# Kernel tuning notes

Measured on AMD Instinct MI355X. Metric: run time of the kernel, lower is better.

Reference implementation:

```python
import jax, jax.numpy as jnp
import numpy as np

B, D, H, E, K = 16384, 1024, 256, 8, 2
EPS = 1e-9


def setup_inputs() -> dict:
    key = jax.random.key(0)
    ks = jax.random.split(key, 4)
    scale_in = 1.0 / np.sqrt(D)
    scale_h = 1.0 / np.sqrt(H)
    return {
        "x": jax.random.normal(ks[0], (B, D), dtype=jnp.float32),
        "gate_w": jax.random.normal(ks[1], (D, E), dtype=jnp.float32) * scale_in,
        "gate_b": jnp.zeros((E,), dtype=jnp.float32),
        "w1": jax.random.normal(ks[2], (E, D, H), dtype=jnp.float32) * scale_in,
        "b1": jnp.zeros((E, H), dtype=jnp.float32),
        "w2": jax.random.normal(ks[3], (E, H, D), dtype=jnp.float32) * scale_h,
        "b2": jnp.zeros((E, D), dtype=jnp.float32),
    }


def reference(x, gate_w, gate_b, w1, b1, w2, b2):
    # Gating: logits -> softmax -> top-k mask -> renormalize (top_k_gating)
    logits = x @ gate_w + gate_b                      # [B, E]
    probs = jax.nn.softmax(logits, axis=-1)           # [B, E]
    _, topk_idx = jax.lax.top_k(probs, K)             # [B, K]
    rows = jnp.arange(probs.shape[0])[:, None]
    mask = jnp.zeros_like(probs).at[rows, topk_idx].set(1.0)
    masked = probs * mask
    denom = jnp.clip(jnp.sum(masked, axis=-1, keepdims=True), EPS, None)
    gating_weights = masked / denom                   # [B, E]

    # Dense all-experts MLP: Linear -> GELU(exact) -> Linear, batched over E
    h = jax.nn.gelu(jnp.einsum('bd,edh->beh', x, w1) + b1, approximate=False)  # [B, E, H]
    expert_outs = jnp.einsum('beh,ehd->bed', h, w2) + b2                        # [B, E, D]

    # Gating-weighted sum over experts
    output = jnp.einsum('bed,be->bd', expert_outs, gating_weights)              # [B, D]
    return output
```

## Files before the change

### kernel.cpp

```cpp
#include <hip/hip_runtime.h>
#include <stdint.h>

#define BN 16384
#define DD 1024
#define HH 256
#define EE 8
#define GB 512
#define GR 32

typedef __attribute__((ext_vector_type(8))) short short8;
typedef __attribute__((ext_vector_type(4))) float floatx4;

__device__ __forceinline__ unsigned short f2bf(float f) {
  union { float f; unsigned int i; } v; v.f = f;
  unsigned int x = v.i;
  x += 0x7fffu + ((x >> 16) & 1u);
  return (unsigned short)(x >> 16);
}
__device__ __forceinline__ unsigned int pack2(float a, float b) {
  return (unsigned int)f2bf(a) | ((unsigned int)f2bf(b) << 16);
}
__device__ __forceinline__ float bf2f(unsigned int u16) {
  union { unsigned int i; float f; } v; v.i = u16 << 16; return v.f;
}
__device__ __forceinline__ void async16(const unsigned short* g, unsigned short* l) {
  __builtin_amdgcn_global_load_lds(
      (const __attribute__((address_space(1))) void*)g,
      (__attribute__((address_space(3))) void*)l, 16, 0, 0);
}

__global__ __launch_bounds__(256) void convert_kernel(const float* __restrict__ x,
                                                      unsigned short* __restrict__ xb) {
  size_t idx = ((size_t)blockIdx.x * 256 + threadIdx.x) * 8;
  float4 f0 = *(const float4*)(x + idx);
  float4 f1 = *(const float4*)(x + idx + 4);
  uint4 o;
  o.x = pack2(f0.x, f0.y); o.y = pack2(f0.z, f0.w);
  o.z = pack2(f1.x, f1.y); o.w = pack2(f1.z, f1.w);
  *(uint4*)(xb + idx) = o;
}

__global__ __launch_bounds__(256) void gating_kernel(
    const float* __restrict__ x,
    const float* __restrict__ gate_w,
    const float* __restrict__ gate_b,
    int* __restrict__ rinfo_e, float* __restrict__ rinfo_w,
    int* __restrict__ bhist) {
  __shared__ int hist[EE];
  int tid = threadIdx.x;
  if (tid < EE) hist[tid] = 0;
  __syncthreads();
  int lane = tid & 63, wv = tid >> 6;
#pragma unroll 1
  for (int it = 0; it < GR / 4; it++) {
    int row = blockIdx.x * GR + it * 4 + wv;
    const float4* xr4 = (const float4*)(x + (size_t)row * DD);
    float acc[EE];
#pragma unroll
    for (int e = 0; e < EE; e++) acc[e] = 0.f;
#pragma unroll
    for (int i = 0; i < 4; i++) {
      int d4 = lane + i * 64;
      float4 xv = xr4[d4];
      const float4* gp = (const float4*)gate_w + (size_t)d4 * 8;
      float xs[4] = {xv.x, xv.y, xv.z, xv.w};
#pragma unroll
      for (int j = 0; j < 4; j++) {
        float4 glo = gp[2 * j], ghi = gp[2 * j + 1];
        acc[0] += xs[j] * glo.x; acc[1] += xs[j] * glo.y;
        acc[2] += xs[j] * glo.z; acc[3] += xs[j] * glo.w;
        acc[4] += xs[j] * ghi.x; acc[5] += xs[j] * ghi.y;
        acc[6] += xs[j] * ghi.z; acc[7] += xs[j] * ghi.w;
      }
    }
#pragma unroll
    for (int s = 1; s < 64; s <<= 1) {
#pragma unroll
      for (int e = 0; e < EE; e++) acc[e] += __shfl_xor(acc[e], s, 64);
    }
    if (lane == 0) {
      float lg[EE];
#pragma unroll
      for (int e = 0; e < EE; e++) lg[e] = acc[e] + gate_b[e];
      int i1 = 0;
      for (int e = 1; e < EE; e++) if (lg[e] > lg[i1]) i1 = e;
      int i2 = (i1 == 0) ? 1 : 0;
      for (int e = 0; e < EE; e++) if (e != i1 && lg[e] > lg[i2]) i2 = e;
      float wA = 1.f / (1.f + __expf(lg[i2] - lg[i1]));
      float wB = 1.f - wA;
      rinfo_e[row] = i1 | (i2 << 8);
      rinfo_w[row * 2 + 0] = wA;
      rinfo_w[row * 2 + 1] = wB;
      atomicAdd(&hist[i1], 1);
      atomicAdd(&hist[i2], 1);
    }
  }
  __syncthreads();
  if (tid < EE) bhist[blockIdx.x * EE + tid] = hist[tid];
}

__global__ __launch_bounds__(256) void scan_kernel(
    const int* __restrict__ bhist, int* __restrict__ cnt, int* __restrict__ bbase) {
  __shared__ int cs[32][EE];
  __shared__ int ofs[EE];
  int tid = threadIdx.x;
  int g = tid & 7, c = tid >> 3;
  int s = 0;
#pragma unroll 1
  for (int b = c * 16; b < c * 16 + 16; b++) s += bhist[b * EE + g];
  cs[c][g] = s;
  __syncthreads();
  if (tid == 0) {
    int run = 0;
    for (int gg = 0; gg < EE; gg++) {
      int tot = 0;
      for (int cc = 0; cc < 32; cc++) tot += cs[cc][gg];
      cnt[gg] = tot;
      cnt[32 + gg] = run;
      ofs[gg] = run;
      run += tot;
    }
  }
  __syncthreads();
  if (tid < EE) {
    int run = ofs[tid];
#pragma unroll 1
    for (int cc = 0; cc < 32; cc++) { int t = cs[cc][tid]; cs[cc][tid] = run; run += t; }
  }
  __syncthreads();
  int run = cs[c][g];
#pragma unroll 1
  for (int b = c * 16; b < c * 16 + 16; b++) {
    bbase[b * EE + g] = run;
    run += bhist[b * EE + g];
  }
}

__global__ __launch_bounds__(64) void scatter_kernel(
    const int* __restrict__ rinfo_e, const float* rinfo_w,
    const int* __restrict__ bbase,
    int* __restrict__ rowidx, float* __restrict__ wgt, int* posmap) {
  __shared__ int curs[EE];
  int tid = threadIdx.x;
  if (tid < EE) curs[tid] = bbase[blockIdx.x * EE + tid];
  __syncthreads();
  if (tid < GR) {
    int row = blockIdx.x * GR + tid;
    int ee = rinfo_e[row];
    int e0 = ee & 255, e1 = (ee >> 8) & 255;
    float w0 = rinfo_w[row * 2 + 0];
    float w1 = rinfo_w[row * 2 + 1];
    int p0 = atomicAdd(&curs[e0], 1);
    rowidx[p0] = row; wgt[p0] = w0;
    int p1 = atomicAdd(&curs[e1], 1);
    rowidx[p1] = row; wgt[p1] = w1;
    posmap[row * 2 + 0] = p0;
    posmap[row * 2 + 1] = p1;
  }
}

__global__ void transpose_kernel(const float* __restrict__ src,
                                 unsigned short* __restrict__ dst, int R, int C) {
  __shared__ float tbuf[32][33];
  int e = blockIdx.z;
  int c0 = blockIdx.x * 32, r0 = blockIdx.y * 32;
  int tx = threadIdx.x, ty = threadIdx.y;
  const float* s = src + (size_t)e * R * C;
  unsigned short* d = dst + (size_t)e * R * C;
  for (int yy = ty; yy < 32; yy += 8)
    tbuf[yy][tx] = s[(size_t)(r0 + yy) * C + c0 + tx];
  __syncthreads();
  for (int yy = ty; yy < 32; yy += 8)
    d[(size_t)(c0 + yy) * R + r0 + tx] = f2bf(tbuf[tx][yy]);
}

template <bool ASYNC_A>
__global__ __launch_bounds__(256) void gemm1_kernel(
    const unsigned short* __restrict__ xb,
    const float* __restrict__ x,
    const unsigned short* __restrict__ w1t,
    const float* __restrict__ b1,
    const int* __restrict__ cnt,
    const int* __restrict__ rowidx,
    unsigned short* __restrict__ hbuf,
    int g0, int g1) {
  __shared__ unsigned short As[128 * 64];
  __shared__ unsigned short Bs[128 * 64];
  int t = blockIdx.x, g = -1, lt = 0;
#pragma unroll 1
  for (int gg = g0; gg < g1; gg++) {
    int nt = (cnt[gg] + 127) >> 7;
    if (t < nt) { g = gg; lt = t; break; }
    t -= nt;
  }
  if (g < 0) return;
  const int* offs = cnt + 32;
  int hb = offs[g0];
  int m0 = offs[g] + lt * 128;
  int mEnd = offs[g] + cnt[g];
  int e = g;
  int n0 = blockIdx.y * 128;
  const unsigned short* Bsrc = w1t + (size_t)e * HH * DD + (size_t)n0 * DD;
  int tid = threadIdx.x, lane = tid & 63, wv = tid >> 6;
  int wr = (wv >> 1) * 64, wc = (wv & 1) * 64;
  int lm = lane & 15, q = lane >> 4;
  floatx4 acc[4][4];
  floatx4 zero = {0.f, 0.f, 0.f, 0.f};
#pragma unroll
  for (int i = 0; i < 4; i++)
#pragma unroll
    for (int j = 0; j < 4; j++) acc[i][j] = zero;
  int srow = tid >> 3;
  int scol = (tid & 7) * 8;
  const unsigned short* gA[4];
  const float* gAf[4];
  const unsigned short* gBp[4];
#pragma unroll
  for (int i = 0; i < 4; i++) {
    int pos = m0 + i * 32 + srow;
    int grow = rowidx[pos < mEnd ? pos : m0];
    if (ASYNC_A) gA[i] = xb + (size_t)grow * DD + scol;
    else         gAf[i] = x + (size_t)grow * DD + scol;
    gBp[i] = Bsrc + (size_t)(i * 32 + srow) * DD + scol;
  }
  unsigned short* AsW = As + wv * 512;
  unsigned short* BsW = Bs + wv * 512;
#pragma unroll 1
  for (int k0 = 0; k0 < DD; k0 += 64) {
    if (ASYNC_A) {
#pragma unroll
      for (int i = 0; i < 4; i++) async16(gA[i], AsW + i * 2048);
#pragma unroll
      for (int i = 0; i < 4; i++) gA[i] += 64;
    } else {
#pragma unroll
      for (int i = 0; i < 4; i++) {
        float4 f0 = *(const float4*)gAf[i];
        float4 f1 = *(const float4*)(gAf[i] + 4);
        gAf[i] += 64;
        uint4 av;
        av.x = pack2(f0.x, f0.y); av.y = pack2(f0.z, f0.w);
        av.z = pack2(f1.x, f1.y); av.w = pack2(f1.z, f1.w);
        *(uint4*)&As[(i * 32 + srow) * 64 + scol] = av;
      }
    }
#pragma unroll
    for (int i = 0; i < 4; i++) async16(gBp[i], BsW + i * 2048);
#pragma unroll
    for (int i = 0; i < 4; i++) gBp[i] += 64;
    __syncthreads();
#pragma unroll
    for (int ks = 0; ks < 2; ks++) {
      short8 a[4], b[4];
#pragma unroll
      for (int i = 0; i < 4; i++)
        a[i] = *(const short8*)&As[(wr + i * 16 + lm) * 64 + ks * 32 + q * 8];
#pragma unroll
      for (int j = 0; j < 4; j++)
        b[j] = *(const short8*)&Bs[(wc + j * 16 + lm) * 64 + ks * 32 + q * 8];
#pragma unroll
      for (int i = 0; i < 4; i++)
#pragma unroll
        for (int j = 0; j < 4; j++)
          acc[i][j] = __builtin_amdgcn_mfma_f32_16x16x32_bf16(b[j], a[i], acc[i][j], 0, 0, 0);
    }
    __syncthreads();
  }
#pragma unroll
  for (int i = 0; i < 4; i++) {
    int pos = m0 + wr + i * 16 + lm;
    if (pos < mEnd) {
#pragma unroll
      for (int j = 0; j < 4; j++) {
        int col = n0 + wc + j * 16 + q * 4;
        const float4 bb = *(const float4*)(b1 + e * HH + col);
        float v0 = acc[i][j][0] + bb.x;
        float v1 = acc[i][j][1] + bb.y;
        float v2 = acc[i][j][2] + bb.z;
        float v3 = acc[i][j][3] + bb.w;
        v0 = 0.5f * v0 * (1.f + erff(v0 * 0.70710678118654752f));
        v1 = 0.5f * v1 * (1.f + erff(v1 * 0.70710678118654752f));
        v2 = 0.5f * v2 * (1.f + erff(v2 * 0.70710678118654752f));
        v3 = 0.5f * v3 * (1.f + erff(v3 * 0.70710678118654752f));
        uint2 st; st.x = pack2(v0, v1); st.y = pack2(v2, v3);
        *(uint2*)(hbuf + (size_t)(pos - hb) * HH + col) = st;
      }
    }
  }
}

template <bool EO>
__global__ __launch_bounds__(256) void gemm2_kernel(
    const unsigned short* __restrict__ hbuf,
    const unsigned short* __restrict__ w2t,
    const float* __restrict__ b2,
    const int* __restrict__ cnt,
    const int* __restrict__ rowidx,
    const float* __restrict__ wgt,
    unsigned short* __restrict__ eo,
    float* out,
    int g0, int g1) {
  __shared__ unsigned short As[128 * 64];
  __shared__ unsigned short Bs[128 * 64];
  int t = blockIdx.x, g = -1, lt = 0;
#pragma unroll 1
  for (int gg = g0; gg < g1; gg++) {
    int nt = (cnt[gg] + 127) >> 7;
    if (t < nt) { g = gg; lt = t; break; }
    t -= nt;
  }
  if (g < 0) return;
  const int* offs = cnt + 32;
  int hb = offs[g0];
  int m0 = offs[g] + lt * 128;
  int mEnd = offs[g] + cnt[g];
  int e = g;
  int n0 = blockIdx.y * 128;
  const unsigned short* Bsrc = w2t + (size_t)e * DD * HH + (size_t)n0 * HH;
  int tid = threadIdx.x, lane = tid & 63, wv = tid >> 6;
  int wr = (wv >> 1) * 64, wc = (wv & 1) * 64;
  int lm = lane & 15, q = lane >> 4;
  floatx4 acc[4][4];
  floatx4 zero = {0.f, 0.f, 0.f, 0.f};
#pragma unroll
  for (int i = 0; i < 4; i++)
#pragma unroll
    for (int j = 0; j < 4; j++) acc[i][j] = zero;
  int srow = tid >> 3;
  int scol = (tid & 7) * 8;
  const unsigned short* gA[4];
  const unsigned short* gBp[4];
#pragma unroll
  for (int i = 0; i < 4; i++) {
    int pos = m0 + i * 32 + srow;
    int posc = (pos < mEnd) ? pos : m0;
    gA[i] = hbuf + (size_t)(posc - hb) * HH + scol;
    gBp[i] = Bsrc + (size_t)(i * 32 + srow) * HH + scol;
  }
  unsigned short* AsW = As + wv * 512;
  unsigned short* BsW = Bs + wv * 512;
#pragma unroll 1
  for (int k0 = 0; k0 < HH; k0 += 64) {
#pragma unroll
    for (int i = 0; i < 4; i++) async16(gA[i], AsW + i * 2048);
#pragma unroll
    for (int i = 0; i < 4; i++) async16(gBp[i], BsW + i * 2048);
#pragma unroll
    for (int i = 0; i < 4; i++) { gA[i] += 64; gBp[i] += 64; }
    __syncthreads();
#pragma unroll
    for (int ks = 0; ks < 2; ks++) {
      short8 a[4], b[4];
#pragma unroll
      for (int i = 0; i < 4; i++)
        a[i] = *(const short8*)&As[(wr + i * 16 + lm) * 64 + ks * 32 + q * 8];
#pragma unroll
      for (int j = 0; j < 4; j++)
        b[j] = *(const short8*)&Bs[(wc + j * 16 + lm) * 64 + ks * 32 + q * 8];
#pragma unroll
      for (int i = 0; i < 4; i++)
#pragma unroll
        for (int j = 0; j < 4; j++)
          acc[i][j] = __builtin_amdgcn_mfma_f32_16x16x32_bf16(b[j], a[i], acc[i][j], 0, 0, 0);
    }
    __syncthreads();
  }
#pragma unroll
  for (int i = 0; i < 4; i++) {
    int pos = m0 + wr + i * 16 + lm;
    if (pos < mEnd) {
      float wrow = wgt[pos];
      if (EO) {
#pragma unroll
        for (int j = 0; j < 4; j++) {
          int col = n0 + wc + j * 16 + q * 4;
          const float4 bb = *(const float4*)(b2 + e * DD + col);
          uint2 st;
          st.x = pack2((acc[i][j][0] + bb.x) * wrow, (acc[i][j][1] + bb.y) * wrow);
          st.y = pack2((acc[i][j][2] + bb.z) * wrow, (acc[i][j][3] + bb.w) * wrow);
          *(uint2*)(eo + (size_t)pos * DD + col) = st;
        }
      } else {
        int grow = rowidx[pos];
#pragma unroll
        for (int j = 0; j < 4; j++) {
          int col = n0 + wc + j * 16 + q * 4;
          const float4 bb = *(const float4*)(b2 + e * DD + col);
          float* op = out + (size_t)grow * DD + col;
          atomicAdd(op + 0, (acc[i][j][0] + bb.x) * wrow);
          atomicAdd(op + 1, (acc[i][j][1] + bb.y) * wrow);
          atomicAdd(op + 2, (acc[i][j][2] + bb.z) * wrow);
          atomicAdd(op + 3, (acc[i][j][3] + bb.w) * wrow);
        }
      }
    }
  }
}

__global__ __launch_bounds__(256) void combine_kernel(
    const unsigned short* __restrict__ eo, const int* __restrict__ posmap,
    float* __restrict__ out) {
  int row = blockIdx.x * 2 + (threadIdx.x >> 7);
  int t = threadIdx.x & 127;
  int p0 = posmap[row * 2 + 0];
  int p1 = posmap[row * 2 + 1];
  uint4 av = *((const uint4*)(eo + (size_t)p0 * DD) + t);
  uint4 bv = *((const uint4*)(eo + (size_t)p1 * DD) + t);
  unsigned int ua[4] = {av.x, av.y, av.z, av.w};
  unsigned int ub[4] = {bv.x, bv.y, bv.z, bv.w};
  float o[8];
#pragma unroll
  for (int k = 0; k < 4; k++) {
    o[2 * k]     = bf2f(ua[k] & 0xffffu) + bf2f(ub[k] & 0xffffu);
    o[2 * k + 1] = bf2f(ua[k] >> 16)     + bf2f(ub[k] >> 16);
  }
  float* op = out + (size_t)row * DD + t * 8;
  *(float4*)(op)     = make_float4(o[0], o[1], o[2], o[3]);
  *(float4*)(op + 4) = make_float4(o[4], o[5], o[6], o[7]);
}

extern "C" void kernel_launch(void* const* d_in, const int* in_sizes, int n_in,
                              void* d_out, int out_size, void* d_ws, size_t ws_size,
                              hipStream_t stream) {
  (void)in_sizes; (void)n_in; (void)out_size;
  const float* x      = (const float*)d_in[0];
  const float* gate_w = (const float*)d_in[1];
  const float* gate_b = (const float*)d_in[2];
  const float* w1     = (const float*)d_in[3];
  const float* b1     = (const float*)d_in[4];
  const float* w2     = (const float*)d_in[5];
  const float* b2     = (const float*)d_in[6];
  float* out = (float*)d_out;

  char* w = (char*)d_ws;
  int* cnt            = (int*)(w);
  int* rinfo_e        = (int*)(w + 256);
  float* rinfo_w      = (float*)(w + 65792);
  int* posmap         = (int*)(w + 65792);
  int* bhist          = (int*)(w + 196864);
  int* bbase          = (int*)(w + 229632);
  int* rowidx         = (int*)(w + 262400);
  float* wgt          = (float*)(w + 393472);
  unsigned short* w1t = (unsigned short*)(w + 524544);
  unsigned short* w2t = (unsigned short*)(w + 4718848);
  unsigned short* hbuf= (unsigned short*)(w + 8913152);
  unsigned short* xb  = (unsigned short*)(w + 25690368);
  unsigned short* eo  = (unsigned short*)(w + 59244800);
  bool fused  = ws_size >= (size_t)25690368;
  bool use_xb = ws_size >= (size_t)59244800;
  bool use_eo = ws_size >= (size_t)126353664;

  transpose_kernel<<<dim3(HH / 32, DD / 32, EE), dim3(32, 8), 0, stream>>>(w1, w1t, DD, HH);
  transpose_kernel<<<dim3(DD / 32, HH / 32, EE), dim3(32, 8), 0, stream>>>(w2, w2t, HH, DD);
  gating_kernel<<<GB, 256, 0, stream>>>(x, gate_w, gate_b, rinfo_e, rinfo_w, bhist);
  scan_kernel<<<1, 256, 0, stream>>>(bhist, cnt, bbase);
  scatter_kernel<<<GB, 64, 0, stream>>>(rinfo_e, rinfo_w, bbase, rowidx, wgt, posmap);
  if (use_eo) {
    convert_kernel<<<BN * DD / (256 * 8), 256, 0, stream>>>(x, xb);
    gemm1_kernel<true><<<dim3(264, 2), 256, 0, stream>>>(xb, x, w1t, b1, cnt, rowidx, hbuf, 0, 8);
    gemm2_kernel<true><<<dim3(264, 8), 256, 0, stream>>>(hbuf, w2t, b2, cnt, rowidx, wgt, eo, nullptr, 0, 8);
    combine_kernel<<<BN / 2, 256, 0, stream>>>(eo, posmap, out);
  } else if (use_xb) {
    hipMemsetAsync(out, 0, (size_t)BN * DD * 4, stream);
    convert_kernel<<<BN * DD / (256 * 8), 256, 0, stream>>>(x, xb);
    gemm1_kernel<true><<<dim3(264, 2), 256, 0, stream>>>(xb, x, w1t, b1, cnt, rowidx, hbuf, 0, 8);
    gemm2_kernel<false><<<dim3(264, 8), 256, 0, stream>>>(hbuf, w2t, b2, cnt, rowidx, wgt, nullptr, out, 0, 8);
  } else {
    (void)fused;
    hipMemsetAsync(out, 0, (size_t)BN * DD * 4, stream);
    gemm1_kernel<false><<<dim3(264, 2), 256, 0, stream>>>(nullptr, x, w1t, b1, cnt, rowidx, hbuf, 0, 8);
    gemm2_kernel<false><<<dim3(264, 8), 256, 0, stream>>>(hbuf, w2t, b2, cnt, rowidx, wgt, nullptr, out, 0, 8);
  }
}
```

Measured before the change: 315.7 us.

## Fuse bf16 convert into gating, double-buffer gemm1 LDS, XOR-swizzle LDS tiles

The separate fp32-to-bf16 conversion of x is folded into the gating kernel, which already reads x, so one full pass over x is removed. gemm1's async path now double-buffers the A/B shared-memory tiles, issuing the next k-tile's global-to-LDS loads before computing on the current one to overlap load latency with MFMA work. Both GEMMs use an XOR swizzle on the 16-byte column chunk, applied at the global source address and at the LDS read, to reduce bank conflicts. The cost is doubled LDS in gemm1, which may reduce occupancy, plus extra address arithmetic.

```diff
diff --git a/kernel.cpp b/kernel.cpp
--- a/kernel.cpp
+++ b/kernel.cpp
@@ -29,23 +29,13 @@
       (__attribute__((address_space(3))) void*)l, 16, 0, 0);
 }
 
-__global__ __launch_bounds__(256) void convert_kernel(const float* __restrict__ x,
-                                                      unsigned short* __restrict__ xb) {
-  size_t idx = ((size_t)blockIdx.x * 256 + threadIdx.x) * 8;
-  float4 f0 = *(const float4*)(x + idx);
-  float4 f1 = *(const float4*)(x + idx + 4);
-  uint4 o;
-  o.x = pack2(f0.x, f0.y); o.y = pack2(f0.z, f0.w);
-  o.z = pack2(f1.x, f1.y); o.w = pack2(f1.z, f1.w);
-  *(uint4*)(xb + idx) = o;
-}
-
 __global__ __launch_bounds__(256) void gating_kernel(
     const float* __restrict__ x,
     const float* __restrict__ gate_w,
     const float* __restrict__ gate_b,
     int* __restrict__ rinfo_e, float* __restrict__ rinfo_w,
-    int* __restrict__ bhist) {
+    int* __restrict__ bhist,
+    unsigned short* __restrict__ xb) {
   __shared__ int hist[EE];
   int tid = threadIdx.x;
   if (tid < EE) hist[tid] = 0;
@@ -62,6 +52,10 @@
     for (int i = 0; i < 4; i++) {
       int d4 = lane + i * 64;
       float4 xv = xr4[d4];
+      if (xb) {
+        uint2 st; st.x = pack2(xv.x, xv.y); st.y = pack2(xv.z, xv.w);
+        *(uint2*)(xb + (size_t)row * DD + (size_t)d4 * 4) = st;
+      }
       const float4* gp = (const float4*)gate_w + (size_t)d4 * 8;
       float xs[4] = {xv.x, xv.y, xv.z, xv.w};
 #pragma unroll
@@ -184,8 +178,8 @@
     const int* __restrict__ rowidx,
     unsigned short* __restrict__ hbuf,
     int g0, int g1) {
-  __shared__ unsigned short As[128 * 64];
-  __shared__ unsigned short Bs[128 * 64];
+  __shared__ unsigned short As[2][8192];
+  __shared__ unsigned short Bs[2][8192];
   int t = blockIdx.x, g = -1, lt = 0;
 #pragma unroll 1
   for (int gg = g0; gg < g1; gg++) {
@@ -204,6 +198,7 @@
   int tid = threadIdx.x, lane = tid & 63, wv = tid >> 6;
   int wr = (wv >> 1) * 64, wc = (wv & 1) * 64;
   int lm = lane & 15, q = lane >> 4;
+  int lm7 = lm & 7;
   floatx4 acc[4][4];
   floatx4 zero = {0.f, 0.f, 0.f, 0.f};
 #pragma unroll
@@ -211,7 +206,8 @@
 #pragma unroll
     for (int j = 0; j < 4; j++) acc[i][j] = zero;
   int srow = tid >> 3;
-  int scol = (tid & 7) * 8;
+  int ssrc = (((tid & 7) ^ (srow & 7))) * 8;
+  int sdst = (tid & 7) * 8;
   const unsigned short* gA[4];
   const float* gAf[4];
   const unsigned short* gBp[4];
@@ -219,20 +215,51 @@
   for (int i = 0; i < 4; i++) {
     int pos = m0 + i * 32 + srow;
     int grow = rowidx[pos < mEnd ? pos : m0];
-    if (ASYNC_A) gA[i] = xb + (size_t)grow * DD + scol;
-    else         gAf[i] = x + (size_t)grow * DD + scol;
-    gBp[i] = Bsrc + (size_t)(i * 32 + srow) * DD + scol;
-  }
-  unsigned short* AsW = As + wv * 512;
-  unsigned short* BsW = Bs + wv * 512;
-#pragma unroll 1
-  for (int k0 = 0; k0 < DD; k0 += 64) {
-    if (ASYNC_A) {
-#pragma unroll
-      for (int i = 0; i < 4; i++) async16(gA[i], AsW + i * 2048);
-#pragma unroll
-      for (int i = 0; i < 4; i++) gA[i] += 64;
-    } else {
+    if (ASYNC_A) gA[i] = xb + (size_t)grow * DD + ssrc;
+    else         gAf[i] = x + (size_t)grow * DD + ssrc;
+    gBp[i] = Bsrc + (size_t)(i * 32 + srow) * DD + ssrc;
+  }
+  auto stageAsync = [&](int bufi) {
+#pragma unroll
+    for (int i = 0; i < 4; i++) async16(gA[i], &As[bufi][wv * 512 + i * 2048]);
+#pragma unroll
+    for (int i = 0; i < 4; i++) gA[i] += 64;
+#pragma unroll
+    for (int i = 0; i < 4; i++) async16(gBp[i], &Bs[bufi][wv * 512 + i * 2048]);
+#pragma unroll
+    for (int i = 0; i < 4; i++) gBp[i] += 64;
+  };
+  auto compute = [&](int bufi) {
+#pragma unroll
+    for (int ks = 0; ks < 2; ks++) {
+      short8 a[4], b[4];
+#pragma unroll
+      for (int i = 0; i < 4; i++)
+        a[i] = *(const short8*)&As[bufi][(wr + i * 16 + lm) * 64 + ((ks * 4 + q) ^ lm7) * 8];
+#pragma unroll
+      for (int j = 0; j < 4; j++)
+        b[j] = *(const short8*)&Bs[bufi][(wc + j * 16 + lm) * 64 + ((ks * 4 + q) ^ lm7) * 8];
+#pragma unroll
+      for (int i = 0; i < 4; i++)
+#pragma unroll
+        for (int j = 0; j < 4; j++)
+          acc[i][j] = __builtin_amdgcn_mfma_f32_16x16x32_bf16(b[j], a[i], acc[i][j], 0, 0, 0);
+    }
+  };
+  if (ASYNC_A) {
+    stageAsync(0);
+    __syncthreads();
+    int buf = 0;
+#pragma unroll 1
+    for (int tt = 0; tt < DD / 64; ++tt) {
+      if (tt < DD / 64 - 1) stageAsync(buf ^ 1);
+      compute(buf);
+      __syncthreads();
+      buf ^= 1;
+    }
+  } else {
+#pragma unroll 1
+    for (int k0 = 0; k0 < DD; k0 += 64) {
 #pragma unroll
       for (int i = 0; i < 4; i++) {
         float4 f0 = *(const float4*)gAf[i];
@@ -241,30 +268,16 @@
         uint4 av;
         av.x = pack2(f0.x, f0.y); av.y = pack2(f0.z, f0.w);
         av.z = pack2(f1.x, f1.y); av.w = pack2(f1.z, f1.w);
-        *(uint4*)&As[(i * 32 + srow) * 64 + scol] = av;
+        *(uint4*)&As[0][(i * 32 + srow) * 64 + sdst] = av;
       }
-    }
-#pragma unroll
-    for (int i = 0; i < 4; i++) async16(gBp[i], BsW + i * 2048);
-#pragma unroll
-    for (int i = 0; i < 4; i++) gBp[i] += 64;
-    __syncthreads();
-#pragma unroll
-    for (int ks = 0; ks < 2; ks++) {
-      short8 a[4], b[4];
-#pragma unroll
-      for (int i = 0; i < 4; i++)
-        a[i] = *(const short8*)&As[(wr + i * 16 + lm) * 64 + ks * 32 + q * 8];
-#pragma unroll
-      for (int j = 0; j < 4; j++)
-        b[j] = *(const short8*)&Bs[(wc + j * 16 + lm) * 64 + ks * 32 + q * 8];
-#pragma unroll
-      for (int i = 0; i < 4; i++)
-#pragma unroll
-        for (int j = 0; j < 4; j++)
-          acc[i][j] = __builtin_amdgcn_mfma_f32_16x16x32_bf16(b[j], a[i], acc[i][j], 0, 0, 0);
-    }
-    __syncthreads();
+#pragma unroll
+      for (int i = 0; i < 4; i++) async16(gBp[i], &Bs[0][wv * 512 + i * 2048]);
+#pragma unroll
+      for (int i = 0; i < 4; i++) gBp[i] += 64;
+      __syncthreads();
+      compute(0);
+      __syncthreads();
+    }
   }
 #pragma unroll
   for (int i = 0; i < 4; i++) {
@@ -320,6 +333,7 @@
   int tid = threadIdx.x, lane = tid & 63, wv = tid >> 6;
   int wr = (wv >> 1) * 64, wc = (wv & 1) * 64;
   int lm = lane & 15, q = lane >> 4;
+  int lm7 = lm & 7;
   floatx4 acc[4][4];
   floatx4 zero = {0.f, 0.f, 0.f, 0.f};
 #pragma unroll
@@ -327,15 +341,15 @@
 #pragma unroll
     for (int j = 0; j < 4; j++) acc[i][j] = zero;
   int srow = tid >> 3;
-  int scol = (tid & 7) * 8;
+  int ssrc = (((tid & 7) ^ (srow & 7))) * 8;
   const unsigned short* gA[4];
   const unsigned short* gBp[4];
 #pragma unroll
   for (int i = 0; i < 4; i++) {
     int pos = m0 + i * 32 + srow;
     int posc = (pos < mEnd) ? pos : m0;
-    gA[i] = hbuf + (size_t)(posc - hb) * HH + scol;
-    gBp[i] = Bsrc + (size_t)(i * 32 + srow) * HH + scol;
+    gA[i] = hbuf + (size_t)(posc - hb) * HH + ssrc;
+    gBp[i] = Bsrc + (size_t)(i * 32 + srow) * HH + ssrc;
   }
   unsigned short* AsW = As + wv * 512;
   unsigned short* BsW = Bs + wv * 512;
@@ -353,10 +367,10 @@
       short8 a[4], b[4];
 #pragma unroll
       for (int i = 0; i < 4; i++)
-        a[i] = *(const short8*)&As[(wr + i * 16 + lm) * 64 + ks * 32 + q * 8];
+        a[i] = *(const short8*)&As[(wr + i * 16 + lm) * 64 + ((ks * 4 + q) ^ lm7) * 8];
 #pragma unroll
       for (int j = 0; j < 4; j++)
-        b[j] = *(const short8*)&Bs[(wc + j * 16 + lm) * 64 + ks * 32 + q * 8];
+        b[j] = *(const short8*)&Bs[(wc + j * 16 + lm) * 64 + ((ks * 4 + q) ^ lm7) * 8];
 #pragma unroll
       for (int i = 0; i < 4; i++)
 #pragma unroll
@@ -446,27 +460,24 @@
   unsigned short* hbuf= (unsigned short*)(w + 8913152);
   unsigned short* xb  = (unsigned short*)(w + 25690368);
   unsigned short* eo  = (unsigned short*)(w + 59244800);
-  bool fused  = ws_size >= (size_t)25690368;
   bool use_xb = ws_size >= (size_t)59244800;
   bool use_eo = ws_size >= (size_t)126353664;
 
   transpose_kernel<<<dim3(HH / 32, DD / 32, EE), dim3(32, 8), 0, stream>>>(w1, w1t, DD, HH);
   transpose_kernel<<<dim3(DD / 32, HH / 32, EE), dim3(32, 8), 0, stream>>>(w2, w2t, HH, DD);
-  gating_kernel<<<GB, 256, 0, stream>>>(x, gate_w, gate_b, rinfo_e, rinfo_w, bhist);
+  gating_kernel<<<GB, 256, 0, stream>>>(x, gate_w, gate_b, rinfo_e, rinfo_w, bhist,
+                                        use_xb ? xb : (unsigned short*)nullptr);
   scan_kernel<<<1, 256, 0, stream>>>(bhist, cnt, bbase);
   scatter_kernel<<<GB, 64, 0, stream>>>(rinfo_e, rinfo_w, bbase, rowidx, wgt, posmap);
   if (use_eo) {
-    convert_kernel<<<BN * DD / (256 * 8), 256, 0, stream>>>(x, xb);
     gemm1_kernel<true><<<dim3(264, 2), 256, 0, stream>>>(xb, x, w1t, b1, cnt, rowidx, hbuf, 0, 8);
     gemm2_kernel<true><<<dim3(264, 8), 256, 0, stream>>>(hbuf, w2t, b2, cnt, rowidx, wgt, eo, nullptr, 0, 8);
     combine_kernel<<<BN / 2, 256, 0, stream>>>(eo, posmap, out);
   } else if (use_xb) {
     hipMemsetAsync(out, 0, (size_t)BN * DD * 4, stream);
-    convert_kernel<<<BN * DD / (256 * 8), 256, 0, stream>>>(x, xb);
     gemm1_kernel<true><<<dim3(264, 2), 256, 0, stream>>>(xb, x, w1t, b1, cnt, rowidx, hbuf, 0, 8);
     gemm2_kernel<false><<<dim3(264, 8), 256, 0, stream>>>(hbuf, w2t, b2, cnt, rowidx, wgt, nullptr, out, 0, 8);
   } else {
-    (void)fused;
     hipMemsetAsync(out, 0, (size_t)BN * DD * 4, stream);
     gemm1_kernel<false><<<dim3(264, 2), 256, 0, stream>>>(nullptr, x, w1t, b1, cnt, rowidx, hbuf, 0, 8);
     gemm2_kernel<false><<<dim3(264, 8), 256, 0, stream>>>(hbuf, w2t, b2, cnt, rowidx, wgt, nullptr, out, 0, 8);
```

Result: faster. 298.5 us (-5.4%).
